# Kernel tuning notes

Measured on AMD Instinct MI355X. Metric: run time of the kernel, lower is better.

The kernel has to match this reference:

```python
import math
import jax, jax.numpy as jnp
import numpy as np

N, E, ELG = 10000, 160000, 320000   # nodes, local edges (= line-graph nodes), line-graph edges
D, H = 256, 8                        # ndim == edim, num_heads
DK = D // H


def setup_inputs() -> dict:
    kit = iter(jax.random.split(jax.random.key(0), 64))
    def rn(shape):
        return jax.random.normal(next(kit), shape, jnp.float32)
    def w(i, o):
        return rn((i, o)) * 0.05
    inp = {
        'x': rn((N, D)),
        'local_lgx': rn((E, D)),
        'global_lgx': rn((E, D)),  # unused for graph_view='local' (faithful to source)
        'local_src': jax.random.randint(next(kit), (E,), 0, N, dtype=jnp.int32),
        'local_dst': (jnp.arange(E, dtype=jnp.int32) % N),  # every node has in-edges -> z > 0
        'lg_src': jax.random.randint(next(kit), (ELG,), 0, E, dtype=jnp.int32),
        'lg_dst': (jnp.arange(ELG, dtype=jnp.int32) % E),
        'src_ids': jax.random.randint(next(kit), (E,), 0, N, dtype=jnp.int32),
        'dst_ids': jax.random.randint(next(kit), (E,), 0, N, dtype=jnp.int32),
    }
    for p in ('n', 'e'):
        inp[p + 'Wq'] = w(D, D); inp[p + 'bq'] = jnp.zeros((D,), jnp.float32)
        inp[p + 'Wk'] = w(D, D)
        inp[p + 'Wv'] = w(D, D)
        inp[p + 'Wo'] = w(D, D); inp[p + 'bo'] = jnp.zeros((D,), jnp.float32)
        inp[p + 'ln1g'] = jnp.ones((D,), jnp.float32); inp[p + 'ln1b'] = jnp.zeros((D,), jnp.float32)
        inp[p + 'W1'] = w(D, 4 * D); inp[p + 'b1'] = jnp.zeros((4 * D,), jnp.float32)
        inp[p + 'W2'] = w(4 * D, D); inp[p + 'b2'] = jnp.zeros((D,), jnp.float32)
        inp[p + 'ln2g'] = jnp.ones((D,), jnp.float32); inp[p + 'ln2b'] = jnp.zeros((D,), jnp.float32)
    return inp


def _ln(x, g, b):
    m = x.mean(-1, keepdims=True)
    v = ((x - m) ** 2).mean(-1, keepdims=True)
    return (x - m) * jax.lax.rsqrt(v + 1e-5) * g + b


def _attn(q, k, v, e, src, dst, n):
    # q,k,v: [n,H,DK]; e: [Eg,H,DK] or None; src,dst: [Eg]
    ks = k[src]
    vs = v[src]
    if e is not None:
        ks = ks + e
        vs = vs + e
    # src_dot_dst + scaled_exp (with clamp, as in lgesql)
    score = jnp.exp(jnp.clip((ks * q[dst]).sum(-1) / math.sqrt(DK), -10.0, 10.0))  # [Eg,H]
    wv = jax.ops.segment_sum(vs * score[..., None], dst, num_segments=n)  # [n,H,DK]
    z = jax.ops.segment_sum(score, dst, num_segments=n)                    # [n,H]
    return wv / z[..., None]


def _block(res, o, Wo, bo, g1, b1, W1, bf1, W2, bf2, g2, b2):
    # layernorm(res + affine_o(o)) followed by FFN with residual+layernorm
    h = _ln(res + o @ Wo + bo, g1, b1)
    return _ln(h + jax.nn.relu(h @ W1 + bf1) @ W2 + bf2, g2, b2)


def reference(x, local_lgx, global_lgx, local_src, local_dst, lg_src, lg_dst, src_ids, dst_ids,
              nWq, nbq, nWk, nWv, nWo, nbo, nln1g, nln1b, nW1, nb1, nW2, nb2, nln2g, nln2b,
              eWq, ebq, eWk, eWv, eWo, ebo, eln1g, eln1b, eW1, eb1, eW2, eb2, eln2g, eln2b):
    # ---- node update (RGATLayer, graph_view='local'); feat_drop=0 (eval) ----
    q = (x @ nWq + nbq).reshape(N, H, DK)
    k = (x @ nWk).reshape(N, H, DK)
    v = (x @ nWv).reshape(N, H, DK)
    e = local_lgx.reshape(E, H, DK)  # edim == ndim -> per-head edge features
    o = _attn(q, k, v, e, local_src, local_dst, N).reshape(N, D)
    out_x = _block(x, o, nWo, nbo, nln1g, nln1b, nW1, nb1, nW2, nb2, nln2g, nln2b)
    # ---- edge update (EdgeRGATLayer on line graph lg) ----
    src_x = x[src_ids]
    dst_x = x[dst_ids]
    qe = (local_lgx @ eWq + ebq + src_x).reshape(E, H, DK)
    ke = (local_lgx @ eWk).reshape(E, H, DK)
    ve = (local_lgx @ eWv + dst_x).reshape(E, H, DK)
    oe = _attn(qe, ke, ve, None, lg_src, lg_dst, E).reshape(E, D)
    out_lgx = _block(local_lgx, oe, eWo, ebo, eln1g, eln1b, eW1, eb1, eW2, eb2, eln2g, eln2b)
    return (out_x, out_lgx)
```

## Files before the change

kernel.cpp:

```cpp
#include <hip/hip_runtime.h>
#include <hip/hip_bf16.h>

typedef __hip_bfloat16 bf16;
typedef __attribute__((ext_vector_type(8))) short short8v;
typedef __attribute__((ext_vector_type(4))) float float4v;

#define N_NODES 10000
#define E_EDGES 160000

__device__ __forceinline__ float b2f(bf16 v){ return __bfloat162float(v); }
__device__ __forceinline__ bf16 f2b(float v){ return __float2bfloat16(v); }

union U8 { int4 v; bf16 h[8]; };
union U4 { int2 v; bf16 h[4]; };

__device__ __forceinline__ float ldx(const void* p, size_t i, bool isb){
    return isb ? b2f(((const bf16*)p)[i]) : ((const float*)p)[i];
}
__device__ __forceinline__ void ld8(const void* p, size_t i, bool isb, float* o){
    if (isb) {
        U8 u; u.v = *reinterpret_cast<const int4*>((const bf16*)p + i);
        #pragma unroll
        for (int j = 0; j < 8; j++) o[j] = b2f(u.h[j]);
    } else {
        const float4* q = reinterpret_cast<const float4*>((const float*)p + i);
        float4 a = q[0], b = q[1];
        o[0]=a.x; o[1]=a.y; o[2]=a.z; o[3]=a.w; o[4]=b.x; o[5]=b.y; o[6]=b.z; o[7]=b.w;
    }
}
__device__ __forceinline__ void stx(void* p, size_t i, bool isb, float v){
    if (isb) ((bf16*)p)[i] = f2b(v); else ((float*)p)[i] = v;
}

typedef const __attribute__((address_space(1))) void* gas_p;
typedef __attribute__((address_space(3))) void* las_p;
__device__ __forceinline__ void gl16(const bf16* g, bf16* l){
    __builtin_amdgcn_global_load_lds((gas_p)g, (las_p)l, 16, 0, 0);
}

__device__ __forceinline__ void quadT(float* a, int t){
    float x0 = (t & 1) ? a[0] : a[1];
    float y0 = __shfl_xor(x0, 1);
    if (t & 1) a[0] = y0; else a[1] = y0;
    float x1 = (t & 1) ? a[2] : a[3];
    float y1 = __shfl_xor(x1, 1);
    if (t & 1) a[2] = y1; else a[3] = y1;
    float x2 = (t & 2) ? a[0] : a[2];
    float y2 = __shfl_xor(x2, 2);
    if (t & 2) a[0] = y2; else a[2] = y2;
    float x3 = (t & 2) ? a[1] : a[3];
    float y3 = __shfl_xor(x3, 2);
    if (t & 2) a[1] = y3; else a[3] = y3;
}

__device__ __forceinline__ int xcd_swz(int wg, int nwg){
    const int q = nwg >> 3, r = nwg & 7;
    const int xcd = wg & 7, ix = wg >> 3;
    return (xcd < r ? xcd * (q + 1) : r * (q + 1) + (xcd - r) * q) + ix;
}

__global__ void detect_dtype(const unsigned short* __restrict__ xw, int* __restrict__ flag){
    const int lane = threadIdx.x;
    int cnt = 0;
    for (int i = lane; i < 8192; i += 64) {
        const unsigned e = (xw[i] >> 7) & 0xFF;
        if (e == 0 || (e >= 100 && e <= 140)) cnt++;
    }
    #pragma unroll
    for (int off = 32; off >= 1; off >>= 1) cnt += __shfl_xor(cnt, off);
    if (lane == 0) *flag = (cnt >= 6554) ? 1 : 0;
}

__global__ __launch_bounds__(256) void cvt_bf16(
    const void* __restrict__ in, bf16* __restrict__ out, long n8, const int* __restrict__ dflag)
{
    const bool isb = (*dflag != 0);
    const long t = (long)blockIdx.x * 256 + threadIdx.x;
    if (t >= n8) return;
    float f[8]; ld8(in, (size_t)t * 8, isb, f);
    U8 u;
    #pragma unroll
    for (int j = 0; j < 8; j++) u.h[j] = f2b(f[j]);
    *reinterpret_cast<int4*>(&out[t * 8]) = u.v;
}

__global__ __launch_bounds__(256) void pack_wT(
    const void* __restrict__ W, bf16* __restrict__ out,
    int K, int Nmat, const int* __restrict__ dflag)
{
    const bool isb = (*dflag != 0);
    const int idx = blockIdx.x * 256 + threadIdx.x;
    if (idx >= K * Nmat) return;
    const int k = idx / Nmat, n = idx - k * Nmat;
    out[(size_t)n * K + k] = f2b(ldx(W, idx, isb));
}

template<int MODE>
__global__ __launch_bounds__(256) void mg(
    const bf16* __restrict__ A, int M, int K, int NC,
    const bf16* __restrict__ Bt0, const bf16* __restrict__ Bt1, const bf16* __restrict__ Bt2,
    const void* __restrict__ bias,
    const bf16* __restrict__ resid,
    const bf16* __restrict__ xg,
    const int* __restrict__ sidx, const int* __restrict__ didx,
    bf16* __restrict__ C, bf16* __restrict__ C2,
    const int* __restrict__ dflag)
{
    const bool isb = (*dflag != 0);
    __shared__ __align__(16) bf16 Al[128 * 64];
    __shared__ __align__(16) bf16 Bl[128 * 64];
    __shared__ float biasl[128];

    const int tid = threadIdx.x;
    const int lane = tid & 63, wave = tid >> 6;
    const int l15 = lane & 15, g = lane >> 4;
    const int t4 = l15 & 3, qd = l15 >> 2;
    const int wr = wave >> 1, wc = wave & 1;

    const int nwgx = gridDim.x;
    int wg = xcd_swz(blockIdx.y * nwgx + blockIdx.x, nwgx * gridDim.y);
    const int rb = (wg / nwgx) * 128, cb = (wg % nwgx) * 128;

    const bf16* Bsel; int cloc;
    if (MODE == 0 || MODE == 7) {
        const int seg = cb >> 8;
        Bsel = (seg == 0) ? Bt0 : ((seg == 1) ? Bt1 : Bt2);
        cloc = cb & 255;
    } else { Bsel = Bt0; cloc = cb; }

    if (tid < 128) {
        float bv = 0.f;
        const int gc = cb + tid;
        if (MODE == 0 || MODE == 7) { if (gc < 256) bv = ldx(bias, gc, isb); }
        else bv = ldx(bias, gc, isb);
        biasl[tid] = bv;
    }

    const int sp = lane & 7, sr8 = lane >> 3;
    int rls[4]; long arows[4];
    #pragma unroll
    for (int j = 0; j < 4; j++) {
        const int rl = wave * 32 + j * 8 + sr8;
        rls[j] = rl;
        const int gm = rb + rl;
        arows[j] = (gm < M) ? gm : (M - 1);
    }

    float4v acc[4][4];
    #pragma unroll
    for (int i = 0; i < 4; i++)
        #pragma unroll
        for (int j = 0; j < 4; j++)
            acc[i][j] = (float4v){0.f, 0.f, 0.f, 0.f};

    for (int k0 = 0; k0 < K; k0 += 64) {
        #pragma unroll
        for (int j = 0; j < 4; j++) {
            const int rl = rls[j];
            const int pp = sp ^ (rl & 7);
            gl16(A + arows[j] * K + k0 + pp * 8,                 Al + rl * 64 + sp * 8);
            gl16(Bsel + (size_t)(cloc + rl) * K + k0 + pp * 8,   Bl + rl * 64 + sp * 8);
        }
        __syncthreads();
        #pragma unroll
        for (int ks = 0; ks < 2; ks++) {
            short8v av[4], bv[4];
            #pragma unroll
            for (int mi = 0; mi < 4; mi++) {
                const int row = wr * 64 + mi * 16 + l15;
                const int cp = (ks * 4 + g) ^ (row & 7);
                av[mi] = *reinterpret_cast<const short8v*>(&Al[row * 64 + cp * 8]);
            }
            #pragma unroll
            for (int ni = 0; ni < 4; ni++) {
                const int row = wc * 64 + ni * 16 + l15;
                const int cp = (ks * 4 + g) ^ (row & 7);
                bv[ni] = *reinterpret_cast<const short8v*>(&Bl[row * 64 + cp * 8]);
            }
            #pragma unroll
            for (int mi = 0; mi < 4; mi++)
                #pragma unroll
                for (int ni = 0; ni < 4; ni++)
                    acc[mi][ni] = __builtin_amdgcn_mfma_f32_16x16x32_bf16(
                        av[mi], bv[ni], acc[mi][ni], 0, 0, 0);
        }
        __syncthreads();
    }

    #pragma unroll
    for (int mi = 0; mi < 4; mi++) {
        const int grow = rb + wr * 64 + mi * 16 + g * 4 + t4;
        const bool ok = (grow < M);
        int s5 = 0, d5 = 0;
        if (MODE == 7 && ok) {
            if (cb < 256) s5 = sidx[grow];
            else if (cb >= 512) d5 = didx[grow];
        }
        #pragma unroll
        for (int ni = 0; ni < 4; ni++) {
            float a[4];
            #pragma unroll
            for (int r = 0; r < 4; r++) a[r] = acc[mi][ni][r];
            quadT(a, t4);
            if (!ok) continue;
            const int ct = wc * 64 + ni * 16 + qd * 4;
            const int gc = cb + ct;
            if (MODE == 0) {
                if (gc < 256) {
                    #pragma unroll
                    for (int u = 0; u < 4; u++) a[u] += biasl[ct + u];
                }
            }
            if (MODE == 3) {
                #pragma unroll
                for (int u = 0; u < 4; u++) a[u] = fmaxf(a[u] + biasl[ct + u], 0.f);
            }
            if (MODE == 7) {
                if (gc < 256) {
                    U4 xx; xx.v = *reinterpret_cast<const int2*>(&xg[(size_t)s5 * 256 + gc]);
                    #pragma unroll
                    for (int u = 0; u < 4; u++) a[u] += biasl[ct + u] + b2f(xx.h[u]);
                } else if (gc >= 512) {
                    U4 xx; xx.v = *reinterpret_cast<const int2*>(&xg[(size_t)d5 * 256 + (gc - 512)]);
                    #pragma unroll
                    for (int u = 0; u < 4; u++) a[u] += b2f(xx.h[u]);
                }
            }
            U4 o;
            #pragma unroll
            for (int u = 0; u < 4; u++) o.h[u] = f2b(a[u]);
            if (MODE == 7) {
                if (gc < 256) *reinterpret_cast<int2*>(&C[(size_t)grow * 256 + gc]) = o.v;
                else          *reinterpret_cast<int2*>(&C2[(size_t)grow * 512 + (gc - 256)]) = o.v;
            } else {
                *reinterpret_cast<int2*>(&C[(size_t)grow * NC + gc]) = o.v;
            }
        }
    }
}

template<int MODE>
__global__ __launch_bounds__(512) void mgln(
    const bf16* __restrict__ A, int M, int K,
    const bf16* __restrict__ Bt,
    const void* __restrict__ bias,
    const bf16* __restrict__ resid,
    const void* __restrict__ lng, const void* __restrict__ lnb,
    bf16* __restrict__ C, void* __restrict__ outv, long obase,
    const int* __restrict__ dflag)
{
    const bool isb = (*dflag != 0);
    __shared__ __align__(16) bf16 Al[128 * 64];
    __shared__ __align__(16) bf16 Bl[256 * 64];
    __shared__ float biasl[256];
    __shared__ float lngl[256];
    __shared__ float lnbl[256];

    const int tid = threadIdx.x;
    const int lane = tid & 63, wave = tid >> 6;
    const int l15 = lane & 15, g = lane >> 4;
    const int t4 = l15 & 3, qd = l15 >> 2;
    const int wr = wave >> 2, wc = wave & 3;

    const int wg = xcd_swz(blockIdx.y, gridDim.y);
    const int rb = wg * 128;

    if (tid < 256) {
        biasl[tid] = ldx(bias, tid, isb);
        lngl[tid]  = ldx(lng,  tid, isb);
        lnbl[tid]  = ldx(lnb,  tid, isb);
    }

    const int sp = lane & 7, sr8 = lane >> 3;
    int rlA[2]; long arA[2];
    #pragma unroll
    for (int j = 0; j < 2; j++) {
        const int rl = wave * 16 + j * 8 + sr8;
        rlA[j] = rl;
        const int gm = rb + rl;
        arA[j] = (gm < M) ? gm : (M - 1);
    }
    int rlB[4];
    #pragma unroll
    for (int j = 0; j < 4; j++) rlB[j] = wave * 32 + j * 8 + sr8;

    float4v acc[4][4];
    #pragma unroll
    for (int i = 0; i < 4; i++)
        #pragma unroll
        for (int j = 0; j < 4; j++)
            acc[i][j] = (float4v){0.f, 0.f, 0.f, 0.f};

    for (int k0 = 0; k0 < K; k0 += 64) {
        #pragma unroll
        for (int j = 0; j < 2; j++) {
            const int pp = sp ^ (rlA[j] & 7);
            gl16(A + arA[j] * K + k0 + pp * 8, Al + rlA[j] * 64 + sp * 8);
        }
        #pragma unroll
        for (int j = 0; j < 4; j++) {
            const int pp = sp ^ (rlB[j] & 7);
            gl16(Bt + (size_t)rlB[j] * K + k0 + pp * 8, Bl + rlB[j] * 64 + sp * 8);
        }
        __syncthreads();
        #pragma unroll
        for (int ks = 0; ks < 2; ks++) {
            short8v av[4], bv[4];
            #pragma unroll
            for (int mi = 0; mi < 4; mi++) {
                const int row = wr * 64 + mi * 16 + l15;
                const int cp = (ks * 4 + g) ^ (row & 7);
                av[mi] = *reinterpret_cast<const short8v*>(&Al[row * 64 + cp * 8]);
            }
            #pragma unroll
            for (int ni = 0; ni < 4; ni++) {
                const int row = wc * 64 + ni * 16 + l15;
                const int cp = (ks * 4 + g) ^ (row & 7);
                bv[ni] = *reinterpret_cast<const short8v*>(&Bl[row * 64 + cp * 8]);
            }
            #pragma unroll
            for (int mi = 0; mi < 4; mi++)
                #pragma unroll
                for (int ni = 0; ni < 4; ni++)
                    acc[mi][ni] = __builtin_amdgcn_mfma_f32_16x16x32_bf16(
                        av[mi], bv[ni], acc[mi][ni], 0, 0, 0);
        }
        __syncthreads();
    }

    float s1[4] = {0.f,0.f,0.f,0.f}, s2[4] = {0.f,0.f,0.f,0.f};
    #pragma unroll
    for (int mi = 0; mi < 4; mi++) {
        const int grow = rb + wr * 64 + mi * 16 + g * 4 + t4;
        const bool ok = (grow < M);
        #pragma unroll
        for (int ni = 0; ni < 4; ni++) {
            float a[4];
            #pragma unroll
            for (int r = 0; r < 4; r++) a[r] = acc[mi][ni][r];
            quadT(a, t4);
            const int ct = wc * 64 + ni * 16 + qd * 4;
            U4 rr; rr.v = make_int2(0, 0);
            if (ok) rr.v = *reinterpret_cast<const int2*>(&resid[(size_t)grow * 256 + ct]);
            #pragma unroll
            for (int u = 0; u < 4; u++) {
                a[u] += biasl[ct + u] + b2f(rr.h[u]);
                s1[mi] += a[u];
                s2[mi] += a[u] * a[u];
                acc[mi][ni][u] = a[u];
            }
        }
    }
    float* Ps1 = (float*)Al;
    float* Ps2 = Ps1 + 2048;
    #pragma unroll
    for (int mi = 0; mi < 4; mi++) {
        const int rowl = wr * 64 + mi * 16 + g * 4 + t4;
        Ps1[(wc * 4 + qd) * 128 + rowl] = s1[mi];
        Ps2[(wc * 4 + qd) * 128 + rowl] = s2[mi];
    }
    __syncthreads();
    float* Mr  = (float*)Bl;
    float* Rsd = Mr + 128;
    if (tid < 128) {
        float a1 = 0.f, a2 = 0.f;
        #pragma unroll
        for (int k = 0; k < 16; k++) { a1 += Ps1[k * 128 + tid]; a2 += Ps2[k * 128 + tid]; }
        const float mn = a1 * (1.f / 256.f);
        const float var = a2 * (1.f / 256.f) - mn * mn;
        Mr[tid] = mn;
        Rsd[tid] = rsqrtf(fmaxf(var, 0.f) + 1e-5f);
    }
    __syncthreads();
    #pragma unroll
    for (int mi = 0; mi < 4; mi++) {
        const int rowl = wr * 64 + mi * 16 + g * 4 + t4;
        const int grow = rb + rowl;
        if (grow >= M) continue;
        const float mn = Mr[rowl], rd = Rsd[rowl];
        #pragma unroll
        for (int ni = 0; ni < 4; ni++) {
            const int ct = wc * 64 + ni * 16 + qd * 4;
            float o[4];
            #pragma unroll
            for (int u = 0; u < 4; u++)
                o[u] = (acc[mi][ni][u] - mn) * rd * lngl[ct + u] + lnbl[ct + u];
            if (MODE == 8) {
                U4 ob;
                #pragma unroll
                for (int u = 0; u < 4; u++) ob.h[u] = f2b(o[u]);
                *reinterpret_cast<int2*>(&C[(size_t)grow * 256 + ct]) = ob.v;
            } else {
                if (isb) {
                    U4 ob;
                    #pragma unroll
                    for (int u = 0; u < 4; u++) ob.h[u] = f2b(o[u]);
                    *reinterpret_cast<int2*>((bf16*)outv + obase + (size_t)grow * 256 + ct) = ob.v;
                } else {
                    float4 f4 = make_float4(o[0], o[1], o[2], o[3]);
                    *reinterpret_cast<float4*>((float*)outv + obase + (size_t)grow * 256 + ct) = f4;
                }
            }
        }
    }
}

__global__ __launch_bounds__(256) void attn_node(
    const bf16* __restrict__ QKV, const int* __restrict__ lsrc,
    const bf16* __restrict__ lgx16, bf16* __restrict__ O)
{
    const int w = threadIdx.x >> 6, lane = threadIdx.x & 63;
    const int d = blockIdx.x * 4 + w;
    if (d >= N_NODES) return;
    const int c4 = lane * 4;
    U4 uq; uq.v = *reinterpret_cast<const int2*>(&QKV[(size_t)d * 768 + c4]);
    float q[4];
    #pragma unroll
    for (int u = 0; u < 4; u++) q[u] = b2f(uq.h[u]);
    float acc[4] = {0.f, 0.f, 0.f, 0.f};
    float z = 0.f;
    for (int j = 0; j < 16; j++) {
        const int i = d + j * N_NODES;
        const int s = lsrc[i];
        U4 ue; ue.v = *reinterpret_cast<const int2*>(&lgx16[(size_t)i * 256 + c4]);
        U4 uk; uk.v = *reinterpret_cast<const int2*>(&QKV[(size_t)s * 768 + 256 + c4]);
        U4 uv; uv.v = *reinterpret_cast<const int2*>(&QKV[(size_t)s * 768 + 512 + c4]);
        float e[4], p = 0.f;
        #pragma unroll
        for (int u = 0; u < 4; u++) {
            e[u] = b2f(ue.h[u]);
            p += (b2f(uk.h[u]) + e[u]) * q[u];
        }
        p += __shfl_xor(p, 4); p += __shfl_xor(p, 2); p += __shfl_xor(p, 1);
        const float sc = expf(fminf(fmaxf(p * 0.17677669529663687f, -10.f), 10.f));
        #pragma unroll
        for (int u = 0; u < 4; u++) acc[u] += (b2f(uv.h[u]) + e[u]) * sc;
        z += sc;
    }
    U4 o;
    const float iz = 1.f / z;
    #pragma unroll
    for (int u = 0; u < 4; u++) o.h[u] = f2b(acc[u] * iz);
    *reinterpret_cast<int2*>(&O[(size_t)d * 256 + c4]) = o.v;
}

__global__ __launch_bounds__(256) void attn_edge_f(
    const bf16* __restrict__ QE, const bf16* __restrict__ KVE,
    const int* __restrict__ lgsrc, bf16* __restrict__ O, int r0, int rows)
{
    const int w = threadIdx.x >> 6, lane = threadIdx.x & 63;
    const int b = blockIdx.x * 4 + w;
    if (b >= rows) return;
    const int dst = r0 + b;
    const int c4 = lane * 4;
    U4 uq; uq.v = *reinterpret_cast<const int2*>(&QE[(size_t)dst * 256 + c4]);
    float q[4];
    #pragma unroll
    for (int u = 0; u < 4; u++) q[u] = b2f(uq.h[u]);
    float acc[4] = {0.f, 0.f, 0.f, 0.f};
    float z = 0.f;
    #pragma unroll
    for (int j = 0; j < 2; j++) {
        const int s = lgsrc[dst + j * E_EDGES];
        const size_t kr = (size_t)s * 512;
        U4 uk; uk.v = *reinterpret_cast<const int2*>(&KVE[kr + c4]);
        U4 uv; uv.v = *reinterpret_cast<const int2*>(&KVE[kr + 256 + c4]);
        float p = 0.f;
        #pragma unroll
        for (int u = 0; u < 4; u++) p += b2f(uk.h[u]) * q[u];
        p += __shfl_xor(p, 4); p += __shfl_xor(p, 2); p += __shfl_xor(p, 1);
        const float sc = expf(fminf(fmaxf(p * 0.17677669529663687f, -10.f), 10.f));
        #pragma unroll
        for (int u = 0; u < 4; u++) acc[u] += b2f(uv.h[u]) * sc;
        z += sc;
    }
    U4 o;
    const float iz = 1.f / z;
    #pragma unroll
    for (int u = 0; u < 4; u++) o.h[u] = f2b(acc[u] * iz);
    *reinterpret_cast<int2*>(&O[(size_t)b * 256 + c4]) = o.v;
}

extern "C" void kernel_launch(void* const* d_in, const int* in_sizes, int n_in,
                              void* d_out, int out_size, void* d_ws, size_t ws_size,
                              hipStream_t stream)
{
    const void* x   = d_in[0];
    const void* lgx = d_in[1];
    const int* local_src = (const int*)d_in[3];
    const int* lg_src    = (const int*)d_in[5];
    const int* src_ids   = (const int*)d_in[7];
    const int* dst_ids   = (const int*)d_in[8];

    const void *nWq = d_in[9],  *nbq = d_in[10], *nWk = d_in[11], *nWv = d_in[12],
               *nWo = d_in[13], *nbo = d_in[14], *nln1g = d_in[15], *nln1b = d_in[16],
               *nW1 = d_in[17], *nb1 = d_in[18], *nW2 = d_in[19], *nb2 = d_in[20],
               *nln2g = d_in[21], *nln2b = d_in[22];
    const void *eWq = d_in[23], *ebq = d_in[24], *eWk = d_in[25], *eWv = d_in[26],
               *eWo = d_in[27], *ebo = d_in[28], *eln1g = d_in[29], *eln1b = d_in[30],
               *eW1 = d_in[31], *eb1 = d_in[32], *eW2 = d_in[33], *eb2 = d_in[34],
               *eln2g = d_in[35], *eln2b = d_in[36];

    const dim3 blk(256);
    const dim3 blk2(512);

    int* dflag = (int*)d_ws;
    detect_dtype<<<1, 64, 0, stream>>>((const unsigned short*)x, dflag);

    bf16* pk = (bf16*)((char*)d_ws + 256);
    bf16 *pnWq = pk,            *pnWk = pk + 65536,   *pnWv = pk + 131072,
         *pnWo = pk + 196608,   *pnW1 = pk + 262144,  *pnW2 = pk + 524288,
         *peWq = pk + 786432,   *peWk = pk + 851968,  *peWv = pk + 917504,
         *peWo = pk + 983040,   *peW1 = pk + 1048576, *peW2 = pk + 1310720;
    bf16* x16   = pk + 1572864;
    bf16* lgx16 = x16 + (size_t)N_NODES * 256;

    cvt_bf16<<<1250,  blk, 0, stream>>>(x,   x16,   (long)N_NODES * 32, dflag);
    cvt_bf16<<<20000, blk, 0, stream>>>(lgx, lgx16, (long)E_EDGES * 32, dflag);

    pack_wT<<<256,  blk, 0, stream>>>(nWq, pnWq, 256, 256,  dflag);
    pack_wT<<<256,  blk, 0, stream>>>(nWk, pnWk, 256, 256,  dflag);
    pack_wT<<<256,  blk, 0, stream>>>(nWv, pnWv, 256, 256,  dflag);
    pack_wT<<<256,  blk, 0, stream>>>(nWo, pnWo, 256, 256,  dflag);
    pack_wT<<<1024, blk, 0, stream>>>(nW1, pnW1, 256, 1024, dflag);
    pack_wT<<<1024, blk, 0, stream>>>(nW2, pnW2, 1024, 256, dflag);
    pack_wT<<<256,  blk, 0, stream>>>(eWq, peWq, 256, 256,  dflag);
    pack_wT<<<256,  blk, 0, stream>>>(eWk, peWk, 256, 256,  dflag);
    pack_wT<<<256,  blk, 0, stream>>>(eWv, peWv, 256, 256,  dflag);
    pack_wT<<<256,  blk, 0, stream>>>(eWo, peWo, 256, 256,  dflag);
    pack_wT<<<1024, blk, 0, stream>>>(eW1, peW1, 256, 1024, dflag);
    pack_wT<<<1024, blk, 0, stream>>>(eW2, peW2, 1024, 256, dflag);

    bf16* QKVN = (bf16*)((char*)d_out + (size_t)N_NODES * 256 * 4);
    bf16* ON   = QKVN + (size_t)N_NODES * 768;
    bf16* HN   = ON   + (size_t)N_NODES * 256;
    bf16* FN   = HN   + (size_t)N_NODES * 256;

    const int gx = (N_NODES + 127) / 128;
    mg<0><<<dim3(6, gx), blk, 0, stream>>>(x16, N_NODES, 256, 768,
        pnWq, pnWk, pnWv, nbq, nullptr, nullptr, nullptr, nullptr,
        QKVN, nullptr, dflag);
    attn_node<<<(N_NODES + 3) / 4, blk, 0, stream>>>(QKVN, local_src, lgx16, ON);
    mgln<8><<<dim3(1, gx), blk2, 0, stream>>>(ON, N_NODES, 256,
        pnWo, nbo, x16, nln1g, nln1b, HN, nullptr, 0, dflag);
    mg<3><<<dim3(8, gx), blk, 0, stream>>>(HN, N_NODES, 256, 1024,
        pnW1, nullptr, nullptr, nb1, nullptr, nullptr, nullptr, nullptr,
        FN, nullptr, dflag);
    mgln<9><<<dim3(1, gx), blk2, 0, stream>>>(FN, N_NODES, 1024,
        pnW2, nb2, HN, nln2g, nln2b, nullptr, d_out, 0, dflag);

    const size_t hdr = 256 + 3145728 + (size_t)5120000 + (size_t)81920000;
    bf16* KVE = (bf16*)((char*)d_ws + hdr);
    bf16* QE  = KVE + (size_t)E_EDGES * 512;
    char* arena = (char*)(QE + (size_t)E_EDGES * 256);

    const size_t used = hdr + (size_t)E_EDGES * 768 * 2;
    long CH = (long)(((ws_size > used ? ws_size - used : 0) / 3072) / 128 * 128);
    if (CH > E_EDGES) CH = E_EDGES;
    if (CH < 128) CH = 128;

    bf16* OE = (bf16*)arena;
    bf16* HE = OE + (size_t)CH * 256;
    bf16* FE = HE + (size_t)CH * 256;

    const int ge = (E_EDGES + 127) / 128;
    mg<7><<<dim3(6, ge), blk, 0, stream>>>(lgx16, E_EDGES, 256, 768,
        peWq, peWk, peWv, ebq, nullptr, x16, src_ids, dst_ids,
        QE, KVE, dflag);

    for (long r0 = 0; r0 < E_EDGES; r0 += CH) {
        const int rows = (int)(((E_EDGES - r0) < CH) ? (E_EDGES - r0) : CH);
        const int gm = (rows + 127) / 128;

        attn_edge_f<<<(rows + 3) / 4, blk, 0, stream>>>(QE, KVE, lg_src, OE, (int)r0, rows);
        mgln<8><<<dim3(1, gm), blk2, 0, stream>>>(OE, rows, 256,
            peWo, ebo, lgx16 + (size_t)r0 * 256, eln1g, eln1b, HE, nullptr, 0, dflag);
        mg<3><<<dim3(8, gm), blk, 0, stream>>>(HE, rows, 256, 1024,
            peW1, nullptr, nullptr, eb1, nullptr, nullptr, nullptr, nullptr,
            FE, nullptr, dflag);
        mgln<9><<<dim3(1, gm), blk2, 0, stream>>>(FE, rows, 1024,
            peW2, eb2, HE, eln2g, eln2b, nullptr, d_out,
            (long)N_NODES * 256 + r0 * 256, dflag);
    }
}
```

Measured before the change: 1.032 ms.

## Fuse FFN up-projection, ReLU, down-projection and LayerNorm into one kernel

Replaces the separate W1 GEMM (writing a 1024-wide intermediate) and the W2+residual+LayerNorm kernel with a single kernel. It processes 64-row tiles, computes the hidden activations in 128-column chunks kept in shared memory, and accumulates the W2 output in registers. This removes the global-memory round trip of the large FFN intermediate and allows a larger edge chunk size. The trade-off is that B operands are read directly from global memory with no LDS staging, and the tiles are smaller, so weight reuse and occupancy may suffer.

```diff
diff --git a/kernel.cpp b/kernel.cpp
--- a/kernel.cpp
+++ b/kernel.cpp
@@ -100,7 +100,6 @@
     const bf16* __restrict__ A, int M, int K, int NC,
     const bf16* __restrict__ Bt0, const bf16* __restrict__ Bt1, const bf16* __restrict__ Bt2,
     const void* __restrict__ bias,
-    const bf16* __restrict__ resid,
     const bf16* __restrict__ xg,
     const int* __restrict__ sidx, const int* __restrict__ didx,
     bf16* __restrict__ C, bf16* __restrict__ C2,
@@ -122,17 +121,16 @@
     const int rb = (wg / nwgx) * 128, cb = (wg % nwgx) * 128;
 
     const bf16* Bsel; int cloc;
-    if (MODE == 0 || MODE == 7) {
+    {
         const int seg = cb >> 8;
         Bsel = (seg == 0) ? Bt0 : ((seg == 1) ? Bt1 : Bt2);
         cloc = cb & 255;
-    } else { Bsel = Bt0; cloc = cb; }
+    }
 
     if (tid < 128) {
         float bv = 0.f;
         const int gc = cb + tid;
-        if (MODE == 0 || MODE == 7) { if (gc < 256) bv = ldx(bias, gc, isb); }
-        else bv = ldx(bias, gc, isb);
+        if (gc < 256) bv = ldx(bias, gc, isb);
         biasl[tid] = bv;
     }
 
@@ -211,10 +209,6 @@
                     for (int u = 0; u < 4; u++) a[u] += biasl[ct + u];
                 }
             }
-            if (MODE == 3) {
-                #pragma unroll
-                for (int u = 0; u < 4; u++) a[u] = fmaxf(a[u] + biasl[ct + u], 0.f);
-            }
             if (MODE == 7) {
                 if (gc < 256) {
                     U4 xx; xx.v = *reinterpret_cast<const int2*>(&xg[(size_t)s5 * 256 + gc]);
@@ -239,14 +233,13 @@
     }
 }
 
-template<int MODE>
-__global__ __launch_bounds__(512) void mgln(
+__global__ __launch_bounds__(512) void mgln8(
     const bf16* __restrict__ A, int M, int K,
     const bf16* __restrict__ Bt,
     const void* __restrict__ bias,
     const bf16* __restrict__ resid,
     const void* __restrict__ lng, const void* __restrict__ lnb,
-    bf16* __restrict__ C, void* __restrict__ outv, long obase,
+    bf16* __restrict__ C,
     const int* __restrict__ dflag)
 {
     const bool isb = (*dflag != 0);
@@ -381,25 +374,191 @@
         #pragma unroll
         for (int ni = 0; ni < 4; ni++) {
             const int ct = wc * 64 + ni * 16 + qd * 4;
+            U4 ob;
+            #pragma unroll
+            for (int u = 0; u < 4; u++)
+                ob.h[u] = f2b((acc[mi][ni][u] - mn) * rd * lngl[ct + u] + lnbl[ct + u]);
+            *reinterpret_cast<int2*>(&C[(size_t)grow * 256 + ct]) = ob.v;
+        }
+    }
+}
+
+__global__ __launch_bounds__(256, 3) void mgffn(
+    const bf16* __restrict__ H, int M,
+    const bf16* __restrict__ W1t, const bf16* __restrict__ W2t,
+    const void* __restrict__ b1, const void* __restrict__ b2,
+    const void* __restrict__ lng, const void* __restrict__ lnb,
+    void* __restrict__ outv, long obase,
+    const int* __restrict__ dflag)
+{
+    const bool isb = (*dflag != 0);
+    __shared__ __align__(16) bf16 Al[64 * 256];
+    __shared__ __align__(16) bf16 Pl[64 * 128];
+
+    const int tid = threadIdx.x;
+    const int lane = tid & 63, wave = tid >> 6;
+    const int l15 = lane & 15, g = lane >> 4;
+    const int t4 = l15 & 3, qd = l15 >> 2;
+    const int wc = wave;
+
+    const int wg = xcd_swz(blockIdx.y, gridDim.y);
+    const int rb = wg * 64;
+
+    const int sgr = lane & 31;
+    const int sr2 = lane >> 5;
+    #pragma unroll
+    for (int it = 0; it < 8; it++) {
+        const int rl = wave * 16 + (it & 7) * 2 + sr2;
+        const long ar = (rb + rl < M) ? (rb + rl) : (M - 1);
+        const int pp = sgr ^ (rl & 7);
+        gl16(H + ar * 256 + pp * 8, Al + rl * 256 + sgr * 8);
+    }
+    __syncthreads();
+
+    float4v oacc[4][4];
+    #pragma unroll
+    for (int i = 0; i < 4; i++)
+        #pragma unroll
+        for (int j = 0; j < 4; j++)
+            oacc[i][j] = (float4v){0.f, 0.f, 0.f, 0.f};
+
+    for (int c = 0; c < 8; c++) {
+        float4v pacc[4][2];
+        #pragma unroll
+        for (int i = 0; i < 4; i++)
+            #pragma unroll
+            for (int j = 0; j < 2; j++)
+                pacc[i][j] = (float4v){0.f, 0.f, 0.f, 0.f};
+        #pragma unroll
+        for (int ks = 0; ks < 8; ks++) {
+            short8v af[4], bf_[2];
+            #pragma unroll
+            for (int mi = 0; mi < 4; mi++) {
+                const int row = mi * 16 + l15;
+                const int cp = (ks * 4 + g) ^ (row & 7);
+                af[mi] = *reinterpret_cast<const short8v*>(&Al[row * 256 + cp * 8]);
+            }
+            #pragma unroll
+            for (int ni = 0; ni < 2; ni++) {
+                const int n = c * 128 + wc * 32 + ni * 16 + l15;
+                bf_[ni] = *reinterpret_cast<const short8v*>(&W1t[(size_t)n * 256 + ks * 32 + g * 8]);
+            }
+            #pragma unroll
+            for (int mi = 0; mi < 4; mi++)
+                #pragma unroll
+                for (int ni = 0; ni < 2; ni++)
+                    pacc[mi][ni] = __builtin_amdgcn_mfma_f32_16x16x32_bf16(
+                        af[mi], bf_[ni], pacc[mi][ni], 0, 0, 0);
+        }
+        __syncthreads();
+        #pragma unroll
+        for (int mi = 0; mi < 4; mi++) {
+            const int prow = mi * 16 + g * 4 + t4;
+            #pragma unroll
+            for (int ni = 0; ni < 2; ni++) {
+                float a[4];
+                #pragma unroll
+                for (int r = 0; r < 4; r++) a[r] = pacc[mi][ni][r];
+                quadT(a, t4);
+                const int pc = wc * 32 + ni * 16 + qd * 4;
+                U4 o;
+                #pragma unroll
+                for (int u = 0; u < 4; u++)
+                    o.h[u] = f2b(fmaxf(a[u] + ldx(b1, c * 128 + pc + u, isb), 0.f));
+                const int wgr = (pc >> 3) ^ (prow & 7);
+                *reinterpret_cast<int2*>(&Pl[prow * 128 + wgr * 8 + (pc & 7)]) = o.v;
+            }
+        }
+        __syncthreads();
+        #pragma unroll
+        for (int ks = 0; ks < 4; ks++) {
+            short8v af2[4], bf2[4];
+            #pragma unroll
+            for (int mi = 0; mi < 4; mi++) {
+                const int row = mi * 16 + l15;
+                const int cp = (ks * 4 + g) ^ (row & 7);
+                af2[mi] = *reinterpret_cast<const short8v*>(&Pl[row * 128 + cp * 8]);
+            }
+            #pragma unroll
+            for (int ni = 0; ni < 4; ni++) {
+                const int n = wc * 64 + ni * 16 + l15;
+                bf2[ni] = *reinterpret_cast<const short8v*>(
+                    &W2t[(size_t)n * 1024 + c * 128 + ks * 32 + g * 8]);
+            }
+            #pragma unroll
+            for (int mi = 0; mi < 4; mi++)
+                #pragma unroll
+                for (int ni = 0; ni < 4; ni++)
+                    oacc[mi][ni] = __builtin_amdgcn_mfma_f32_16x16x32_bf16(
+                        af2[mi], bf2[ni], oacc[mi][ni], 0, 0, 0);
+        }
+    }
+    __syncthreads();
+
+    float s1[4] = {0.f,0.f,0.f,0.f}, s2[4] = {0.f,0.f,0.f,0.f};
+    #pragma unroll
+    for (int mi = 0; mi < 4; mi++) {
+        const int rowl = mi * 16 + g * 4 + t4;
+        #pragma unroll
+        for (int ni = 0; ni < 4; ni++) {
+            float a[4];
+            #pragma unroll
+            for (int r = 0; r < 4; r++) a[r] = oacc[mi][ni][r];
+            quadT(a, t4);
+            const int ct = wc * 64 + ni * 16 + qd * 4;
+            const int rg = (ct >> 3) ^ (rowl & 7);
+            U4 rr; rr.v = *reinterpret_cast<const int2*>(&Al[rowl * 256 + rg * 8 + (ct & 7)]);
+            #pragma unroll
+            for (int u = 0; u < 4; u++) {
+                a[u] += ldx(b2, ct + u, isb) + b2f(rr.h[u]);
+                s1[mi] += a[u];
+                s2[mi] += a[u] * a[u];
+                oacc[mi][ni][u] = a[u];
+            }
+        }
+    }
+    float* Ps1 = (float*)Pl;
+    float* Ps2 = Ps1 + 1024;
+    float* Mr  = Ps2 + 1024;
+    float* Rsd = Mr + 64;
+    #pragma unroll
+    for (int mi = 0; mi < 4; mi++) {
+        const int rowl = mi * 16 + g * 4 + t4;
+        Ps1[(wc * 4 + qd) * 64 + rowl] = s1[mi];
+        Ps2[(wc * 4 + qd) * 64 + rowl] = s2[mi];
+    }
+    __syncthreads();
+    if (tid < 64) {
+        float a1 = 0.f, a2 = 0.f;
+        #pragma unroll
+        for (int k = 0; k < 16; k++) { a1 += Ps1[k * 64 + tid]; a2 += Ps2[k * 64 + tid]; }
+        const float mn = a1 * (1.f / 256.f);
+        const float var = a2 * (1.f / 256.f) - mn * mn;
+        Mr[tid] = mn;
+        Rsd[tid] = rsqrtf(fmaxf(var, 0.f) + 1e-5f);
+    }
+    __syncthreads();
+    #pragma unroll
+    for (int mi = 0; mi < 4; mi++) {
+        const int rowl = mi * 16 + g * 4 + t4;
+        const int grow = rb + rowl;
+        if (grow >= M) continue;
+        const float mn = Mr[rowl], rd = Rsd[rowl];
+        #pragma unroll
+        for (int ni = 0; ni < 4; ni++) {
+            const int ct = wc * 64 + ni * 16 + qd * 4;
             float o[4];
             #pragma unroll
             for (int u = 0; u < 4; u++)
-                o[u] = (acc[mi][ni][u] - mn) * rd * lngl[ct + u] + lnbl[ct + u];
-            if (MODE == 8) {
+                o[u] = (oacc[mi][ni][u] - mn) * rd * ldx(lng, ct + u, isb) + ldx(lnb, ct + u, isb);
+            if (isb) {
                 U4 ob;
                 #pragma unroll
                 for (int u = 0; u < 4; u++) ob.h[u] = f2b(o[u]);
-                *reinterpret_cast<int2*>(&C[(size_t)grow * 256 + ct]) = ob.v;
+                *reinterpret_cast<int2*>((bf16*)outv + obase + (size_t)grow * 256 + ct) = ob.v;
             } else {
-                if (isb) {
-                    U4 ob;
-                    #pragma unroll
-                    for (int u = 0; u < 4; u++) ob.h[u] = f2b(o[u]);
-                    *reinterpret_cast<int2*>((bf16*)outv + obase + (size_t)grow * 256 + ct) = ob.v;
-                } else {
-                    float4 f4 = make_float4(o[0], o[1], o[2], o[3]);
-                    *reinterpret_cast<float4*>((float*)outv + obase + (size_t)grow * 256 + ct) = f4;
-                }
+                float4 f4 = make_float4(o[0], o[1], o[2], o[3]);
+                *reinterpret_cast<float4*>((float*)outv + obase + (size_t)grow * 256 + ct) = f4;
             }
         }
     }
@@ -534,20 +693,17 @@
     bf16* QKVN = (bf16*)((char*)d_out + (size_t)N_NODES * 256 * 4);
     bf16* ON   = QKVN + (size_t)N_NODES * 768;
     bf16* HN   = ON   + (size_t)N_NODES * 256;
-    bf16* FN   = HN   + (size_t)N_NODES * 256;
 
     const int gx = (N_NODES + 127) / 128;
+    const int gx64 = (N_NODES + 63) / 64;
     mg<0><<<dim3(6, gx), blk, 0, stream>>>(x16, N_NODES, 256, 768,
-        pnWq, pnWk, pnWv, nbq, nullptr, nullptr, nullptr, nullptr,
+        pnWq, pnWk, pnWv, nbq, nullptr, nullptr, nullptr,
         QKVN, nullptr, dflag);
     attn_node<<<(N_NODES + 3) / 4, blk, 0, stream>>>(QKVN, local_src, lgx16, ON);
-    mgln<8><<<dim3(1, gx), blk2, 0, stream>>>(ON, N_NODES, 256,
-        pnWo, nbo, x16, nln1g, nln1b, HN, nullptr, 0, dflag);
-    mg<3><<<dim3(8, gx), blk, 0, stream>>>(HN, N_NODES, 256, 1024,
-        pnW1, nullptr, nullptr, nb1, nullptr, nullptr, nullptr, nullptr,
-        FN, nullptr, dflag);
-    mgln<9><<<dim3(1, gx), blk2, 0, stream>>>(FN, N_NODES, 1024,
-        pnW2, nb2, HN, nln2g, nln2b, nullptr, d_out, 0, dflag);
+    mgln8<<<dim3(1, gx), blk2, 0, stream>>>(ON, N_NODES, 256,
+        pnWo, nbo, x16, nln1g, nln1b, HN, dflag);
+    mgffn<<<dim3(1, gx64), blk, 0, stream>>>(HN, N_NODES,
+        pnW1, pnW2, nb1, nb2, nln2g, nln2b, d_out, 0, dflag);
 
     const size_t hdr = 256 + 3145728 + (size_t)5120000 + (size_t)81920000;
     bf16* KVE = (bf16*)((char*)d_ws + hdr);
@@ -555,31 +711,28 @@
     char* arena = (char*)(QE + (size_t)E_EDGES * 256);
 
     const size_t used = hdr + (size_t)E_EDGES * 768 * 2;
-    long CH = (long)(((ws_size > used ? ws_size - used : 0) / 3072) / 128 * 128);
+    long CH = (long)(((ws_size > used ? ws_size - used : 0) / 1024) / 128 * 128);
     if (CH > E_EDGES) CH = E_EDGES;
     if (CH < 128) CH = 128;
 
     bf16* OE = (bf16*)arena;
     bf16* HE = OE + (size_t)CH * 256;
-    bf16* FE = HE + (size_t)CH * 256;
 
     const int ge = (E_EDGES + 127) / 128;
     mg<7><<<dim3(6, ge), blk, 0, stream>>>(lgx16, E_EDGES, 256, 768,
-        peWq, peWk, peWv, ebq, nullptr, x16, src_ids, dst_ids,
+        peWq, peWk, peWv, ebq, x16, src_ids, dst_ids,
         QE, KVE, dflag);
 
     for (long r0 = 0; r0 < E_EDGES; r0 += CH) {
         const int rows = (int)(((E_EDGES - r0) < CH) ? (E_EDGES - r0) : CH);
         const int gm = (rows + 127) / 128;
+        const int gm64 = (rows + 63) / 64;
 
         attn_edge_f<<<(rows + 3) / 4, blk, 0, stream>>>(QE, KVE, lg_src, OE, (int)r0, rows);
-        mgln<8><<<dim3(1, gm), blk2, 0, stream>>>(OE, rows, 256,
-            peWo, ebo, lgx16 + (size_t)r0 * 256, eln1g, eln1b, HE, nullptr, 0, dflag);
-        mg<3><<<dim3(8, gm), blk, 0, stream>>>(HE, rows, 256, 1024,
-            peW1, nullptr, nullptr, eb1, nullptr, nullptr, nullptr, nullptr,
-            FE, nullptr, dflag);
-        mgln<9><<<dim3(1, gm), blk2, 0, stream>>>(FE, rows, 1024,
-            peW2, eb2, HE, eln2g, eln2b, nullptr, d_out,
+        mgln8<<<dim3(1, gm), blk2, 0, stream>>>(OE, rows, 256,
+            peWo, ebo, lgx16 + (size_t)r0 * 256, eln1g, eln1b, HE, dflag);
+        mgffn<<<dim3(1, gm64), blk, 0, stream>>>(HE, rows,
+            peW1, peW2, eb1, eb2, eln2g, eln2b, d_out,
             (long)N_NODES * 256 + r0 * 256, dflag);
     }
 }
```

After: 1.216 ms. 17.8% more time.
